# Optimization experiments

Hardware: AMD Instinct MI355X
Metric: run time of the kernel (lower is better)

Reference implementation:

```python
import jax, jax.numpy as jnp
import numpy as np

B, N, K = 32, 1024, 20          # graphs, points per graph, kNN neighbors
EMB = 1024                       # emb_dims
OUT = 7                          # out_channels
WS1, ST1, G1 = 52, 20, 7         # linear1 STFT-KAN: window, stride, gridsize
WS2, ST2, G2 = 197, 7, 6         # linear2 STFT-KAN
NW1 = (128 - WS1) // ST1 + 1     # 4 windows over 128-dim features
NW2 = (2 * EMB - WS2) // ST2 + 1 # 265 windows over 2048-dim features


def _window(kind, M):
    n = jnp.arange(M, dtype=jnp.float32)
    if kind == 'bartlett':
        return 1.0 - jnp.abs(2.0 * n / M - 1.0)        # periodic bartlett (torch default)
    return 0.5 * (1.0 - jnp.cos(2.0 * jnp.pi * n / M)) # periodic hann


def _stft_kan(x, coeffs, bias, gridsize, ws, stride, wtype):
    """x: [B, D]; coeffs: [2, outdim, nw, ws, gridsize]; returns [B, outdim]."""
    D = x.shape[1]
    nw = (D - ws) // stride + 1
    idx = jnp.arange(nw)[:, None] * stride + jnp.arange(ws)[None, :]  # [nw, ws]
    xw = x[:, idx] * _window(wtype, ws)                               # [B, nw, ws]
    kk = jnp.arange(1, gridsize + 1, dtype=x.dtype)
    ang = xw[..., None] * kk                                          # [B, nw, ws, g]
    y = jnp.einsum('bnwg,onwg->bo', jnp.cos(ang), coeffs[0])
    y = y + jnp.einsum('bnwg,onwg->bo', jnp.sin(ang), coeffs[1])
    return y + bias


def setup_inputs() -> dict:
    key = jax.random.key(0)
    ks = jax.random.split(key, 8)
    pos = jax.random.normal(ks[0], (B * N, 3), jnp.float32)
    batch = jnp.repeat(jnp.arange(B, dtype=jnp.int32), N)  # sorted, equal-size graphs
    # EdgeConv MLP([6,64,128]): Linear+BN+ReLU, then plain Linear
    W1 = jax.random.normal(ks[1], (6, 64), jnp.float32) * 0.3
    b1 = jnp.zeros((64,), jnp.float32)
    gamma1 = jnp.ones((64,), jnp.float32)
    beta1 = jnp.zeros((64,), jnp.float32)
    W2 = jax.random.normal(ks[2], (64, 128), jnp.float32) * 0.1
    b2 = jnp.zeros((128,), jnp.float32)
    # STFT-KAN 1 (smooth init: coeffs damped by k^2)
    k1 = np.arange(1, G1 + 1, dtype=np.float32)
    c1 = jax.random.normal(ks[3], (2, EMB, NW1, WS1, G1), jnp.float32) / (np.sqrt(NW1 * WS1) * (k1 ** 2))
    bi1 = jnp.zeros((EMB,), jnp.float32)
    # STFT-KAN 2 (non-smooth init)
    c2 = jax.random.normal(ks[4], (2, OUT, NW2, WS2, G2), jnp.float32) / (np.sqrt(NW2 * WS2) * np.sqrt(G2))
    bi2 = jnp.zeros((OUT,), jnp.float32)
    return {"pos": pos, "batch": batch, "W1": W1, "b1": b1, "gamma1": gamma1,
            "beta1": beta1, "W2": W2, "b2": b2, "c1": c1, "bi1": bi1, "c2": c2, "bi2": bi2}


def reference(pos, batch, W1, b1, gamma1, beta1, W2, b2, c1, bi1, c2, bi2):
    p = pos.reshape(B, N, 3)
    # dynamic kNN graph per batch element (exclude self)
    sq = jnp.sum(p * p, axis=-1)                                    # [B, N]
    d2 = sq[:, :, None] + sq[:, None, :] - 2.0 * jnp.einsum('bnd,bmd->bnm', p, p)
    d2 = d2 + jnp.eye(N, dtype=p.dtype) * 1e10
    _, idx = jax.lax.top_k(-d2, K)                                  # [B, N, K]
    pj = jax.vmap(lambda pts, ids: pts[ids])(p, idx)                # [B, N, K, 3]
    pi = jnp.broadcast_to(p[:, :, None, :], (B, N, K, 3))
    e = jnp.concatenate([pi, pj - pi], axis=-1)                     # [B, N, K, 6]
    # edge MLP: Linear -> BN -> ReLU -> Linear
    h = e @ W1 + b1
    mu = h.mean((0, 1, 2))
    var = h.var((0, 1, 2))
    h = gamma1 * (h - mu) * jax.lax.rsqrt(var + 1e-5) + beta1
    h = jax.nn.relu(h)
    h = h @ W2 + b2                                                 # [B, N, K, 128]
    x1 = h.max(axis=2).reshape(B * N, 128)                          # max aggregation over neighbors
    x = _stft_kan(x1, c1, bi1, G1, WS1, ST1, 'bartlett')            # [B*N, EMB]
    xg = x.reshape(B, N, EMB)
    xcat = jnp.concatenate([xg.max(axis=1), xg.mean(axis=1)], axis=-1)  # global max/mean pool
    return _stft_kan(xcat, c2, bi2, G2, WS2, ST2, 'hann')           # [B, OUT]
```

## Files before the change

kernel.cpp:

```cpp
#include <hip/hip_runtime.h>
#include <cstdint>

typedef _Float16 half8 __attribute__((ext_vector_type(8)));
typedef float f32x4 __attribute__((ext_vector_type(4)));

__device__ __forceinline__ void gload16(const void* g, void* l) {
  __builtin_amdgcn_global_load_lds(
      (const __attribute__((address_space(1))) void*)g,
      (__attribute__((address_space(3))) void*)l, 16, 0, 0);
}

__global__ __launch_bounds__(256) void knn_kernel(const float* __restrict__ pos,
                                                  int* __restrict__ nbr) {
  __shared__ float px[1024], py[1024], pz[1024], sq[1024];
  int tid = threadIdx.x;
  int b = blockIdx.x >> 8;
  const float* pg = pos + (size_t)b * 3072;
  for (int m = 0; m < 4; ++m) {
    int j = m * 256 + tid;
    float x = pg[3 * j], y = pg[3 * j + 1], z = pg[3 * j + 2];
    px[j] = x; py[j] = y; pz[j] = z; sq[j] = x * x + y * y + z * z;
  }
  __syncthreads();
  int wave = tid >> 6, lane = tid & 63;
  int n = (blockIdx.x & 255) * 4 + wave;
  float xi = px[n], yi = py[n], zi = pz[n], si = sq[n];
  float d[16];
#pragma unroll
  for (int i = 0; i < 16; ++i) {
    int j = i * 64 + lane;
    float dd = si + sq[j] - 2.0f * (xi * px[j] + yi * py[j] + zi * pz[j]);
    d[i] = (j == n) ? 1e30f : dd;
  }
  int outbase = (b * 1024 + n) * 20;
  for (int kk = 0; kk < 20; ++kk) {
    float lmin = d[0]; int lpos = 0;
#pragma unroll
    for (int i = 1; i < 16; ++i)
      if (d[i] < lmin) { lmin = d[i]; lpos = i; }
    float bv = lmin; int bi = lpos * 64 + lane;
#pragma unroll
    for (int off = 1; off < 64; off <<= 1) {
      float ov = __shfl_xor(bv, off);
      int   oi = __shfl_xor(bi, off);
      if (ov < bv || (ov == bv && oi < bi)) { bv = ov; bi = oi; }
    }
    if (lane == 0) nbr[outbase + kk] = b * 1024 + bi;
    if ((bi & 63) == lane) {
      int rp = bi >> 6;
#pragma unroll
      for (int i = 0; i < 16; ++i)
        if (i == rp) d[i] = 1e30f;
    }
  }
}

__global__ __launch_bounds__(256) void edge_stats_kernel(
    const float* __restrict__ pos, const int* __restrict__ nbr,
    const float* __restrict__ W1, const float* __restrict__ b1v,
    float* __restrict__ psum, float* __restrict__ psq) {
  __shared__ float els[256][6];
  __shared__ float w1s[384];
  __shared__ float b1s[64];
  __shared__ float red[8][64];
  int tid = threadIdx.x, bid = blockIdx.x;
  for (int f = tid; f < 384; f += 256) w1s[f] = W1[f];
  if (tid < 64) b1s[tid] = b1v[tid];
  int c = tid & 63, grp = tid >> 6;
  float s = 0.f, s2 = 0.f;
  for (int ch = 0; ch < 5; ++ch) {
    int E = bid * 1280 + ch * 256 + tid;
    int p = E / 20;
    int j = nbr[E];
    float pix = pos[3 * p], piy = pos[3 * p + 1], piz = pos[3 * p + 2];
    float e3 = pos[3 * j] - pix, e4 = pos[3 * j + 1] - piy, e5 = pos[3 * j + 2] - piz;
    __syncthreads();
    els[tid][0] = pix; els[tid][1] = piy; els[tid][2] = piz;
    els[tid][3] = e3;  els[tid][4] = e4;  els[tid][5] = e5;
    __syncthreads();
    for (int m = 0; m < 64; ++m) {
      int e = grp * 64 + m;
      float h = b1s[c];
#pragma unroll
      for (int d = 0; d < 6; ++d) h += els[e][d] * w1s[d * 64 + c];
      s += h; s2 += h * h;
    }
  }
  red[grp][c] = s;
  __syncthreads();
  red[4 + grp][c] = s2;
  __syncthreads();
  if (tid < 64) {
    float S = red[0][tid] + red[1][tid] + red[2][tid] + red[3][tid];
    float Q = red[4][tid] + red[5][tid] + red[6][tid] + red[7][tid];
    psum[bid * 64 + tid] = S;
    psq[bid * 64 + tid] = Q;
  }
}

__global__ void bn_finalize_kernel(const float* __restrict__ psum, const float* __restrict__ psq,
                                   const float* __restrict__ gamma, const float* __restrict__ beta,
                                   float* __restrict__ bns, float* __restrict__ bnh) {
  int c = threadIdx.x;
  float s = 0.f, q = 0.f;
  for (int b = 0; b < 512; ++b) { s += psum[b * 64 + c]; q += psq[b * 64 + c]; }
  const float inv = 1.0f / 655360.0f;
  float mu = s * inv;
  float var = q * inv - mu * mu;
  float sc = gamma[c] * rsqrtf(var + 1e-5f);
  bns[c] = sc;
  bnh[c] = beta[c] - mu * sc;
}

__global__ __launch_bounds__(256) void edge_mlp_kernel(
    const float* __restrict__ pos, const int* __restrict__ nbr,
    const float* __restrict__ W1, const float* __restrict__ b1v,
    const float* __restrict__ bns, const float* __restrict__ bnh,
    const float* __restrict__ W2, const float* __restrict__ b2v,
    float* __restrict__ x1) {
  __shared__ __align__(16) char elds[53248];
  _Float16* Ah = (_Float16*)(elds);
  _Float16* Al = (_Float16*)(elds + 10240);
  _Float16* Bh = (_Float16*)(elds + 20480);
  _Float16* Bl = (_Float16*)(elds + 36864);
  float* outb = (float*)elds;
  __shared__ float w1s[384];
  __shared__ float b1s[64], scs[64], shs[64];
  int tid = threadIdx.x, bid = blockIdx.x;
  for (int f = tid; f < 384; f += 256) w1s[f] = W1[f];
  if (tid < 64) { b1s[tid] = b1v[tid]; scs[tid] = bns[tid]; shs[tid] = bnh[tid]; }
#pragma unroll
  for (int i = 0; i < 32; ++i) {
    int flat = tid + 256 * i;
    int dd = flat >> 7, c = flat & 127;
    float v = W2[flat];
    _Float16 hi = (_Float16)v;
    _Float16 lo = (_Float16)(v - (float)hi);
    int byte = c * 128 + ((((dd >> 3) ^ (c & 7))) << 4) + (dd & 7) * 2;
    *(_Float16*)((char*)Bh + byte) = hi;
    *(_Float16*)((char*)Bl + byte) = lo;
  }
  __syncthreads();
#pragma unroll
  for (int m = 0; m < 20; ++m) {
    int flat = tid + 256 * m;
    int row = flat >> 6;
    int d = flat & 63;
    int j = nbr[bid * 80 + row];
    int P = bid * 4 + (row / 20);
    float pix = pos[3 * P], piy = pos[3 * P + 1], piz = pos[3 * P + 2];
    float e3 = pos[3 * j] - pix, e4 = pos[3 * j + 1] - piy, e5 = pos[3 * j + 2] - piz;
    float h = b1s[d];
    h += pix * w1s[d] + piy * w1s[64 + d] + piz * w1s[128 + d]
       + e3 * w1s[192 + d] + e4 * w1s[256 + d] + e5 * w1s[320 + d];
    h = scs[d] * h + shs[d];
    h = fmaxf(h, 0.f);
    _Float16 hi = (_Float16)h;
    _Float16 lo = (_Float16)(h - (float)hi);
    int byte = row * 128 + ((((d >> 3) ^ (row & 7))) << 4) + (d & 7) * 2;
    *(_Float16*)((char*)Ah + byte) = hi;
    *(_Float16*)((char*)Al + byte) = lo;
  }
  __syncthreads();
  int wave = tid >> 6, lane = tid & 63;
  int l15 = lane & 15, l4 = lane >> 4;
  f32x4 acc[5][2] = {};
#pragma unroll
  for (int ks = 0; ks < 2; ++ks) {
    int slotk = ks * 4 + l4;
    half8 bfh[2], bfl[2];
#pragma unroll
    for (int ci = 0; ci < 2; ++ci) {
      int col = (wave * 2 + ci) * 16 + l15;
      int byte = col * 128 + ((slotk ^ (col & 7)) << 4);
      bfh[ci] = *(const half8*)((char*)Bh + byte);
      bfl[ci] = *(const half8*)((char*)Bl + byte);
    }
#pragma unroll
    for (int rt = 0; rt < 5; ++rt) {
      int row = rt * 16 + l15;
      int byte = row * 128 + ((slotk ^ (row & 7)) << 4);
      half8 ah = *(const half8*)((char*)Ah + byte);
      half8 al = *(const half8*)((char*)Al + byte);
#pragma unroll
      for (int ci = 0; ci < 2; ++ci) {
        acc[rt][ci] = __builtin_amdgcn_mfma_f32_16x16x32_f16(ah, bfh[ci], acc[rt][ci], 0, 0, 0);
        acc[rt][ci] = __builtin_amdgcn_mfma_f32_16x16x32_f16(ah, bfl[ci], acc[rt][ci], 0, 0, 0);
        acc[rt][ci] = __builtin_amdgcn_mfma_f32_16x16x32_f16(al, bfh[ci], acc[rt][ci], 0, 0, 0);
      }
    }
  }
  __syncthreads();
#pragma unroll
  for (int rt = 0; rt < 5; ++rt)
#pragma unroll
    for (int ci = 0; ci < 2; ++ci) {
      int col = (wave * 2 + ci) * 16 + l15;
#pragma unroll
      for (int q = 0; q < 4; ++q) {
        int row = rt * 16 + l4 * 4 + q;
        outb[row * 129 + col] = acc[rt][ci][q];
      }
    }
  __syncthreads();
#pragma unroll
  for (int r = 0; r < 2; ++r) {
    int it = tid + 256 * r;
    int p = it >> 7, c = it & 127;
    float mx = -1e30f;
#pragma unroll
    for (int e = 0; e < 20; ++e) mx = fmaxf(mx, outb[(p * 20 + e) * 129 + c]);
    x1[((size_t)bid * 4 + p) * 128 + c] = mx + b2v[c];
  }
}

__global__ void kan1_tables_kernel(int* __restrict__ dimt, float* __restrict__ wkt) {
  int j = blockIdx.x * 256 + threadIdx.x;
  if (j >= 2944) return;
  if (j >= 2912) { dimt[j] = 0; wkt[j] = 0.0f; return; }
  int r = j % 1456;
  int n = r / 364, r2 = r % 364;
  int w = r2 / 7, g = r2 % 7;
  dimt[j] = n * 20 + w;
  float bart = 1.0f - fabsf(2.0f * (float)w / 52.0f - 1.0f);
  wkt[j] = bart * (float)(g + 1);
}

__global__ void c1_to_f16_kernel(const float* __restrict__ c1, _Float16* __restrict__ Cf) {
  int L = blockIdx.x * 256 + threadIdx.x;
  if (L >= 1024 * 2944) return;
  int o = L / 2944, j = L % 2944;
  float v = 0.0f;
  if (j < 2912) {
    int t = j / 1456, r = j % 1456;
    v = c1[(size_t)(t * 1024 + o) * 1456 + r];
  }
  Cf[L] = (_Float16)v;
}

__global__ __launch_bounds__(256, 4) void kan1_gemm_kernel(
    const float* __restrict__ x1, const _Float16* __restrict__ Cf,
    const int* __restrict__ dimt, const float* __restrict__ wkt,
    float* __restrict__ pmax, float* __restrict__ psump) {
  __shared__ __align__(16) _Float16 Asm[128 * 64];
  __shared__ __align__(16) _Float16 Bsm[128 * 64];
  __shared__ int   tdim[2][64];
  __shared__ float twk[2][64];
  int tid = threadIdx.x;
  int bm = blockIdx.x, bn = blockIdx.y;
  int m0 = bm << 7, n0 = bn << 7;
  int wave = tid >> 6, lane = tid & 63;
  int wr = wave >> 1, wc = wave & 1;
  int l15 = lane & 15, l4 = lane >> 4;

  if (tid < 64) { tdim[0][tid] = dimt[tid]; twk[0][tid] = wkt[tid]; }
  f32x4 acc[4][4] = {};
  __syncthreads();

  for (int t = 0; t < 46; ++t) {
    int j0 = t << 6;
#pragma unroll
    for (int i = 0; i < 4; ++i) {
      int idx = i * 256 + tid;
      int col = idx >> 3, slot = idx & 7;
      int sslot = slot ^ (col & 7);
      const _Float16* src = Cf + (size_t)(n0 + col) * 2944 + j0 + sslot * 8;
      gload16(src, (char*)Bsm + idx * 16);
    }
    if (t < 45 && tid < 64) {
      tdim[(t + 1) & 1][tid] = dimt[j0 + 64 + tid];
      twk[(t + 1) & 1][tid] = wkt[j0 + 64 + tid];
    }
    const int* td = tdim[t & 1];
    const float* tw = twk[t & 1];
#pragma unroll
    for (int rep = 0; rep < 4; ++rep) {
      int slot = tid + rep * 256;
      int r = slot >> 3, s = slot & 7;
      const float* xrow = x1 + (size_t)(m0 + r) * 128;
      int d0 = td[s * 8], d7 = td[s * 8 + 7];
      float x0 = xrow[d0], x7 = xrow[d7];
      half8 av;
#pragma unroll
      for (int e = 0; e < 8; ++e) {
        int jj = s * 8 + e;
        float xv = (td[jj] == d0) ? x0 : x7;
        float ph = (j0 + jj >= 1456) ? 1.57079632679489662f : 0.0f;
        av[e] = (_Float16)__cosf(xv * tw[jj] - ph);
      }
      *(half8*)((char*)Asm + r * 128 + ((s ^ (r & 7)) << 4)) = av;
    }
    __syncthreads();
#pragma unroll
    for (int ksub = 0; ksub < 2; ++ksub) {
      int slotk = ksub * 4 + l4;
      half8 bf[4];
#pragma unroll
      for (int ni = 0; ni < 4; ++ni) {
        int col = wc * 64 + ni * 16 + l15;
        bf[ni] = *(const half8*)((char*)Bsm + col * 128 + ((slotk ^ (col & 7)) << 4));
      }
#pragma unroll
      for (int mi = 0; mi < 4; ++mi) {
        int row = wr * 64 + mi * 16 + l15;
        half8 af = *(const half8*)((char*)Asm + row * 128 + ((slotk ^ (row & 7)) << 4));
#pragma unroll
        for (int ni = 0; ni < 4; ++ni)
          acc[mi][ni] = __builtin_amdgcn_mfma_f32_16x16x32_f16(af, bf[ni], acc[mi][ni], 0, 0, 0);
      }
    }
    __syncthreads();
  }

  float* pooled = (float*)Bsm;
#pragma unroll
  for (int ni = 0; ni < 4; ++ni) {
    float mx = -1e30f, sm = 0.f;
#pragma unroll
    for (int mi = 0; mi < 4; ++mi)
#pragma unroll
      for (int q = 0; q < 4; ++q) {
        float v = acc[mi][ni][q];
        mx = fmaxf(mx, v); sm += v;
      }
    mx = fmaxf(mx, __shfl_xor(mx, 16)); sm += __shfl_xor(sm, 16);
    mx = fmaxf(mx, __shfl_xor(mx, 32)); sm += __shfl_xor(sm, 32);
    if (l4 == 0) {
      int col = wc * 64 + ni * 16 + l15;
      pooled[(wr * 2 + 0) * 128 + col] = mx;
      pooled[(wr * 2 + 1) * 128 + col] = sm;
    }
  }
  __syncthreads();
  if (tid < 128) {
    float mx = fmaxf(pooled[tid], pooled[2 * 128 + tid]);
    float sm = pooled[128 + tid] + pooled[3 * 128 + tid];
    pmax[(size_t)bm * 1024 + n0 + tid] = mx;
    psump[(size_t)bm * 1024 + n0 + tid] = sm;
  }
}

__global__ void pool_reduce_kernel(const float* __restrict__ pmax, const float* __restrict__ psump,
                                   const float* __restrict__ bi1,
                                   float* __restrict__ gmax, float* __restrict__ gmean) {
  int gid = blockIdx.x * 256 + threadIdx.x;
  int b = gid >> 10, col = gid & 1023;
  float mx = -1e30f, sm = 0.f;
  for (int t = 0; t < 8; ++t) {
    mx = fmaxf(mx, pmax[(size_t)(b * 8 + t) * 1024 + col]);
    sm += psump[(size_t)(b * 8 + t) * 1024 + col];
  }
  float bias = bi1[col];
  gmax[gid] = mx + bias;
  gmean[gid] = sm * (1.0f / 1024.0f) + bias;
}

__global__ __launch_bounds__(256) void kan2_kernel(
    const float* __restrict__ gmax, const float* __restrict__ gmean,
    const float* __restrict__ c2, float* __restrict__ part) {
  __shared__ float xc[2048];
  __shared__ float hw[197];
  __shared__ float racc[7][256];
  int b = blockIdx.x, s = blockIdx.y, tid = threadIdx.x;
  for (int f = tid; f < 1024; f += 256) {
    xc[f] = gmax[b * 1024 + f];
    xc[1024 + f] = gmean[b * 1024 + f];
  }
  for (int f = tid; f < 197; f += 256)
    hw[f] = 0.5f * (1.0f - cosf(6.283185307179586f * (float)f / 197.0f));
  float acc[7] = {};
  __syncthreads();
  int qlo = (52205 * s) / 16, qhi = (52205 * (s + 1)) / 16;
  for (int q = qlo + tid; q < qhi; q += 256) {
    int n = q / 197;
    int w = q - n * 197;
    float xw = xc[n * 7 + w] * hw[w];
    float s1, c1v;
    __sincosf(xw, &s1, &c1v);
    float ckv[6], skv[6];
    {
      float ck = c1v, sk = s1;
#pragma unroll
      for (int g = 0; g < 6; ++g) {
        ckv[g] = ck; skv[g] = sk;
        float cn = ck * c1v - sk * s1;
        sk = sk * c1v + ck * s1;
        ck = cn;
      }
    }
    int base = q * 6;
#pragma unroll
    for (int o = 0; o < 7; ++o) {
      const float* pc = c2 + (size_t)o * 313230 + base;
      const float* ps = c2 + (size_t)(o + 7) * 313230 + base;
      float sc = 0.f, ss = 0.f;
#pragma unroll
      for (int g = 0; g < 6; ++g) { sc += ckv[g] * pc[g]; ss += skv[g] * ps[g]; }
      acc[o] += sc + ss;
    }
  }
#pragma unroll
  for (int o = 0; o < 7; ++o) racc[o][tid] = acc[o];
  __syncthreads();
  for (int st = 128; st >= 1; st >>= 1) {
    if (tid < st)
#pragma unroll
      for (int o = 0; o < 7; ++o) racc[o][tid] += racc[o][tid + st];
    __syncthreads();
  }
  if (tid < 7) part[(b * 16 + s) * 7 + tid] = racc[tid][0];
}

__global__ void kan2_reduce_kernel(const float* __restrict__ part, const float* __restrict__ bi2,
                                   float* __restrict__ out) {
  int i = threadIdx.x;
  if (i >= 224) return;
  int b = i / 7, o = i % 7;
  float s = 0.f;
  for (int t = 0; t < 16; ++t) s += part[(b * 16 + t) * 7 + o];
  out[b * 7 + o] = s + bi2[o];
}

extern "C" void kernel_launch(void* const* d_in, const int* in_sizes, int n_in,
                              void* d_out, int out_size, void* d_ws, size_t ws_size,
                              hipStream_t stream) {
  const float* pos    = (const float*)d_in[0];
  const float* W1     = (const float*)d_in[2];
  const float* b1     = (const float*)d_in[3];
  const float* gamma1 = (const float*)d_in[4];
  const float* beta1  = (const float*)d_in[5];
  const float* W2     = (const float*)d_in[6];
  const float* b2     = (const float*)d_in[7];
  const float* c1     = (const float*)d_in[8];
  const float* bi1    = (const float*)d_in[9];
  const float* c2     = (const float*)d_in[10];
  const float* bi2    = (const float*)d_in[11];
  float* out = (float*)d_out;
  char* ws = (char*)d_ws;

  int*      nbr   = (int*)     (ws + 0);
  float*    x1    = (float*)   (ws + 2621440);
  _Float16* Cf    = (_Float16*)(ws + 19398656);
  int*      dimt  = (int*)     (ws + 25427968);
  float*    wkt   = (float*)   (ws + 25439744);
  float*    psum  = (float*)   (ws + 25451520);
  float*    psq   = (float*)   (ws + 25582592);
  float*    bns   = (float*)   (ws + 25713664);
  float*    bnh   = (float*)   (ws + 25713920);
  float*    pmax  = (float*)   (ws + 25714176);
  float*    psump = (float*)   (ws + 26762752);
  float*    gmax  = (float*)   (ws + 27811328);
  float*    gmean = (float*)   (ws + 27942400);
  float*    part  = (float*)   (ws + 28073472);
  if (ws_size < 28087808) return;

  knn_kernel<<<8192, 256, 0, stream>>>(pos, nbr);
  kan1_tables_kernel<<<12, 256, 0, stream>>>(dimt, wkt);
  c1_to_f16_kernel<<<11776, 256, 0, stream>>>(c1, Cf);
  edge_stats_kernel<<<512, 256, 0, stream>>>(pos, nbr, W1, b1, psum, psq);
  bn_finalize_kernel<<<1, 64, 0, stream>>>(psum, psq, gamma1, beta1, bns, bnh);
  edge_mlp_kernel<<<8192, 256, 0, stream>>>(pos, nbr, W1, b1, bns, bnh, W2, b2, x1);
  kan1_gemm_kernel<<<dim3(256, 8), 256, 0, stream>>>(x1, Cf, dimt, wkt, pmax, psump);
  pool_reduce_kernel<<<128, 256, 0, stream>>>(pmax, psump, bi1, gmax, gmean);
  kan2_kernel<<<dim3(32, 16), 256, 0, stream>>>(gmax, gmean, c2, part);
  kan2_reduce_kernel<<<1, 256, 0, stream>>>(part, bi2, out);
}
```

Baseline: 660.8 us.

## Double-buffer KAN1 GEMM and widen tile to 128x256 with 512 threads

```diff
diff --git a/kernel.cpp b/kernel.cpp
--- a/kernel.cpp
+++ b/kernel.cpp
@@ -238,44 +238,39 @@
   Cf[L] = (_Float16)v;
 }
 
-__global__ __launch_bounds__(256, 4) void kan1_gemm_kernel(
+__global__ __launch_bounds__(512, 2) void kan1_gemm_kernel(
     const float* __restrict__ x1, const _Float16* __restrict__ Cf,
     const int* __restrict__ dimt, const float* __restrict__ wkt,
     float* __restrict__ pmax, float* __restrict__ psump) {
-  __shared__ __align__(16) _Float16 Asm[128 * 64];
-  __shared__ __align__(16) _Float16 Bsm[128 * 64];
+  __shared__ __align__(16) _Float16 Asm[2][128 * 64];
+  __shared__ __align__(16) _Float16 Bsm[2][256 * 64];
   __shared__ int   tdim[2][64];
   __shared__ float twk[2][64];
   int tid = threadIdx.x;
   int bm = blockIdx.x, bn = blockIdx.y;
-  int m0 = bm << 7, n0 = bn << 7;
+  int m0 = bm << 7, n0 = bn << 8;
   int wave = tid >> 6, lane = tid & 63;
-  int wr = wave >> 1, wc = wave & 1;
+  int wr = wave >> 2, wc = wave & 3;
   int l15 = lane & 15, l4 = lane >> 4;
 
-  if (tid < 64) { tdim[0][tid] = dimt[tid]; twk[0][tid] = wkt[tid]; }
-  f32x4 acc[4][4] = {};
-  __syncthreads();
-
-  for (int t = 0; t < 46; ++t) {
+  auto stageB = [&](int t, int nb) {
     int j0 = t << 6;
 #pragma unroll
     for (int i = 0; i < 4; ++i) {
-      int idx = i * 256 + tid;
+      int idx = i * 512 + tid;
       int col = idx >> 3, slot = idx & 7;
       int sslot = slot ^ (col & 7);
-      const _Float16* src = Cf + (size_t)(n0 + col) * 2944 + j0 + sslot * 8;
-      gload16(src, (char*)Bsm + idx * 16);
-    }
-    if (t < 45 && tid < 64) {
-      tdim[(t + 1) & 1][tid] = dimt[j0 + 64 + tid];
-      twk[(t + 1) & 1][tid] = wkt[j0 + 64 + tid];
-    }
+      gload16(Cf + (size_t)(n0 + col) * 2944 + j0 + sslot * 8,
+              (char*)Bsm[nb] + idx * 16);
+    }
+  };
+  auto agen = [&](int t, int nb) {
     const int* td = tdim[t & 1];
     const float* tw = twk[t & 1];
-#pragma unroll
-    for (int rep = 0; rep < 4; ++rep) {
-      int slot = tid + rep * 256;
+    int j0 = t << 6;
+#pragma unroll
+    for (int rep = 0; rep < 2; ++rep) {
+      int slot = tid + rep * 512;
       int r = slot >> 3, s = slot & 7;
       const float* xrow = x1 + (size_t)(m0 + r) * 128;
       int d0 = td[s * 8], d7 = td[s * 8 + 7];
@@ -288,31 +283,52 @@
         float ph = (j0 + jj >= 1456) ? 1.57079632679489662f : 0.0f;
         av[e] = (_Float16)__cosf(xv * tw[jj] - ph);
       }
-      *(half8*)((char*)Asm + r * 128 + ((s ^ (r & 7)) << 4)) = av;
-    }
-    __syncthreads();
+      *(half8*)((char*)Asm[nb] + r * 128 + ((s ^ (r & 7)) << 4)) = av;
+    }
+  };
+
+  if (tid < 64)                { tdim[0][tid]      = dimt[tid];            twk[0][tid]      = wkt[tid]; }
+  else if (tid < 128)          { tdim[1][tid - 64] = dimt[tid];            twk[1][tid - 64] = wkt[tid]; }
+  f32x4 acc[4][4] = {};
+  __syncthreads();
+  stageB(0, 0);
+  agen(0, 0);
+  __syncthreads();
+
+  for (int t = 0; t < 46; ++t) {
+    int cur = t & 1, nxt = cur ^ 1;
+    if (t < 45) stageB(t + 1, nxt);
+    half8 af[2][4], bf[2][4];
 #pragma unroll
     for (int ksub = 0; ksub < 2; ++ksub) {
       int slotk = ksub * 4 + l4;
-      half8 bf[4];
+#pragma unroll
+      for (int mi = 0; mi < 4; ++mi) {
+        int row = wr * 64 + mi * 16 + l15;
+        af[ksub][mi] = *(const half8*)((char*)Asm[cur] + row * 128 + ((slotk ^ (row & 7)) << 4));
+      }
 #pragma unroll
       for (int ni = 0; ni < 4; ++ni) {
         int col = wc * 64 + ni * 16 + l15;
-        bf[ni] = *(const half8*)((char*)Bsm + col * 128 + ((slotk ^ (col & 7)) << 4));
-      }
-#pragma unroll
-      for (int mi = 0; mi < 4; ++mi) {
-        int row = wr * 64 + mi * 16 + l15;
-        half8 af = *(const half8*)((char*)Asm + row * 128 + ((slotk ^ (row & 7)) << 4));
+        bf[ksub][ni] = *(const half8*)((char*)Bsm[cur] + col * 128 + ((slotk ^ (col & 7)) << 4));
+      }
+    }
+    if (t < 45) agen(t + 1, nxt);
+    if (t < 44 && tid < 64) {
+      tdim[cur][tid] = dimt[(t + 2) * 64 + tid];
+      twk[cur][tid]  = wkt[(t + 2) * 64 + tid];
+    }
+#pragma unroll
+    for (int ksub = 0; ksub < 2; ++ksub)
+#pragma unroll
+      for (int mi = 0; mi < 4; ++mi)
 #pragma unroll
         for (int ni = 0; ni < 4; ++ni)
-          acc[mi][ni] = __builtin_amdgcn_mfma_f32_16x16x32_f16(af, bf[ni], acc[mi][ni], 0, 0, 0);
-      }
-    }
+          acc[mi][ni] = __builtin_amdgcn_mfma_f32_16x16x32_f16(af[ksub][mi], bf[ksub][ni], acc[mi][ni], 0, 0, 0);
     __syncthreads();
   }
 
-  float* pooled = (float*)Bsm;
+  float* pooled = (float*)Asm;
 #pragma unroll
   for (int ni = 0; ni < 4; ++ni) {
     float mx = -1e30f, sm = 0.f;
@@ -327,14 +343,14 @@
     mx = fmaxf(mx, __shfl_xor(mx, 32)); sm += __shfl_xor(sm, 32);
     if (l4 == 0) {
       int col = wc * 64 + ni * 16 + l15;
-      pooled[(wr * 2 + 0) * 128 + col] = mx;
-      pooled[(wr * 2 + 1) * 128 + col] = sm;
-    }
-  }
-  __syncthreads();
-  if (tid < 128) {
-    float mx = fmaxf(pooled[tid], pooled[2 * 128 + tid]);
-    float sm = pooled[128 + tid] + pooled[3 * 128 + tid];
+      pooled[(wr * 2 + 0) * 256 + col] = mx;
+      pooled[(wr * 2 + 1) * 256 + col] = sm;
+    }
+  }
+  __syncthreads();
+  if (tid < 256) {
+    float mx = fmaxf(pooled[tid], pooled[512 + tid]);
+    float sm = pooled[256 + tid] + pooled[768 + tid];
     pmax[(size_t)bm * 1024 + n0 + tid] = mx;
     psump[(size_t)bm * 1024 + n0 + tid] = sm;
   }
@@ -460,7 +476,7 @@
   edge_stats_kernel<<<512, 256, 0, stream>>>(pos, nbr, W1, b1, psum, psq);
   bn_finalize_kernel<<<1, 64, 0, stream>>>(psum, psq, gamma1, beta1, bns, bnh);
   edge_mlp_kernel<<<8192, 256, 0, stream>>>(pos, nbr, W1, b1, bns, bnh, W2, b2, x1);
-  kan1_gemm_kernel<<<dim3(256, 8), 256, 0, stream>>>(x1, Cf, dimt, wkt, pmax, psump);
+  kan1_gemm_kernel<<<dim3(256, 4), 512, 0, stream>>>(x1, Cf, dimt, wkt, pmax, psump);
   pool_reduce_kernel<<<128, 256, 0, stream>>>(pmax, psump, bi1, gmax, gmean);
   kan2_kernel<<<dim3(32, 16), 256, 0, stream>>>(gmax, gmean, c2, part);
   kan2_reduce_kernel<<<1, 256, 0, stream>>>(part, bi2, out);
```

Result: faster. 601.5 us (-9.0%).
